# Kernel optimization log

Measured on AMD Instinct MI355X. Metric: run time of the kernel, lower is better.

The kernel has to match this reference:

```python
import jax, jax.numpy as jnp
import numpy as np

B, T, L, D, H = 8, 8192, 256, 512, 8
HD = D // H  # head_dim = 64


def setup_inputs() -> dict:
    key = jax.random.key(0)
    ks = jax.random.split(key, 6)
    s = 0.02
    return {
        "x": jax.random.normal(ks[0], (B, T, D), jnp.float32),
        "query": jax.random.normal(ks[1], (B, L, D), jnp.float32),
        "Wq": jax.random.normal(ks[2], (D, D), jnp.float32) * s,
        "bq": jnp.zeros((D,), jnp.float32),
        "Wkv": jax.random.normal(ks[3], (D, 2 * D), jnp.float32) * s,
        "bkv": jnp.zeros((2 * D,), jnp.float32),
        "Wproj": jax.random.normal(ks[4], (D, D), jnp.float32) * s,
        "bproj": jnp.zeros((D,), jnp.float32),
    }


def reference(x, query, Wq, bq, Wkv, bkv, Wproj, bproj):
    scale = HD ** (-0.5)
    # projections (weights stored [in, out]; equivalent to torch Linear with W.T)
    q = (query @ Wq + bq).reshape(B, L, H, HD).transpose(0, 2, 1, 3)   # [B,H,L,hd]
    kv = (x @ Wkv + bkv).reshape(B, T, 2, H, HD)
    k = kv[:, :, 0].transpose(0, 2, 1, 3)                              # [B,H,T,hd]
    v = kv[:, :, 1].transpose(0, 2, 1, 3)                              # [B,H,T,hd]
    # scaled dot-product attention, full L x T scores as in original
    attn = jnp.einsum("bhld,bhtd->bhlt", q * scale, k)                 # [B,H,L,T]
    attn = jax.nn.softmax(attn, axis=-1)
    out = jnp.einsum("bhlt,bhtd->bhld", attn, v)                       # [B,H,L,hd]
    out = out.transpose(0, 2, 1, 3).reshape(B, L, D)
    return out @ Wproj + bproj
```

## Files before the change

kernel.cpp:

```cpp
#include <hip/hip_runtime.h>
#include <hip/hip_bf16.h>
#include <cstdint>
#include <cstddef>

typedef __bf16 bf16_t;
typedef __bf16 bf16x8 __attribute__((ext_vector_type(8)));
typedef __bf16 bf16x4 __attribute__((ext_vector_type(4)));
typedef float  f32x4  __attribute__((ext_vector_type(4)));

#define DEVI __device__ __forceinline__

constexpr int B_ = 8, T_ = 8192, L_ = 256, D_ = 512, H_ = 8, HD_ = 64;
constexpr float SCALE_LOG2E = 0.125f * 1.44269504088896340736f;
constexpr int NSPLIT = 8;

DEVI void async16(void* lds_base, const void* gptr, int lane) {
#if __has_builtin(__builtin_amdgcn_global_load_lds)
  __builtin_amdgcn_global_load_lds(
      (__attribute__((address_space(1))) void*)gptr,
      (__attribute__((address_space(3))) void*)lds_base, 16, 0, 0);
  (void)lane;
#else
  ((bf16x8*)lds_base)[lane] = *(const bf16x8*)gptr;
#endif
}

__global__ __launch_bounds__(256) void cvt_f32_to_bf16(
    const float* __restrict__ in, bf16_t* __restrict__ out, int n4) {
  int stride = gridDim.x * blockDim.x;
  for (int i = blockIdx.x * blockDim.x + threadIdx.x; i < n4; i += stride) {
    float4 v = ((const float4*)in)[i];
    bf16x4 o;
    o[0] = (bf16_t)v.x; o[1] = (bf16_t)v.y; o[2] = (bf16_t)v.z; o[3] = (bf16_t)v.w;
    ((bf16x4*)out)[i] = o;
  }
}

__global__ __launch_bounds__(256) void transpose_cvt(
    const float* __restrict__ W, bf16_t* __restrict__ WT, int K, int N, float scale) {
  __shared__ float tile[32][33];
  const int tx = threadIdx.x & 31, ty = threadIdx.x >> 5;
  const int n0 = blockIdx.x * 32, k0 = blockIdx.y * 32;
#pragma unroll
  for (int i = 0; i < 4; ++i)
    tile[ty + i * 8][tx] = W[(size_t)(k0 + ty + i * 8) * N + n0 + tx];
  __syncthreads();
#pragma unroll
  for (int i = 0; i < 4; ++i)
    WT[(size_t)(n0 + ty + i * 8) * K + k0 + tx] = (bf16_t)(tile[tx][ty + i * 8] * scale);
}

template <int MODE>
__global__ __launch_bounds__(256, 2) void gemm_bf16(
    const bf16_t* __restrict__ A, const bf16_t* __restrict__ BT,
    const float* __restrict__ bias, float bscale,
    bf16_t* __restrict__ out0, bf16_t* __restrict__ out1,
    float* __restrict__ outf) {
  constexpr int K = 512;
  __shared__ __align__(16) bf16_t As[128 * 32];
  __shared__ __align__(16) bf16_t Bs[128 * 32];
  __shared__ __align__(16) bf16_t Cs[128 * 136];

  const int tid = threadIdx.x;
  const int w = tid >> 6, lane = tid & 63;
  const int m0 = (MODE == 1 ? blockIdx.y : blockIdx.x) * 128;
  const int n0 = (MODE == 1 ? blockIdx.x : blockIdx.y) * 128;
  const int wm = w & 1, wn = w >> 1;

  f32x4 acc[4][4] = {};

  const int srow = w * 32 + (lane >> 2);
  const int scol = (lane & 3) * 8;
  const bf16_t* aG = A + (size_t)(m0 + srow) * K + scol;
  const bf16_t* bG = BT + (size_t)(n0 + srow) * K + scol;
  bf16_t* aL = &As[(w * 32) * 32];
  bf16_t* bL = &Bs[(w * 32) * 32];

  for (int k0 = 0; k0 < K; k0 += 32) {
    async16(aL,           aG + k0,                 lane);
    async16(aL + 16 * 32, aG + k0 + (size_t)16 * K, lane);
    async16(bL,           bG + k0,                 lane);
    async16(bL + 16 * 32, bG + k0 + (size_t)16 * K, lane);
    __syncthreads();
    bf16x8 af[4], bfr[4];
#pragma unroll
    for (int mt = 0; mt < 4; ++mt)
      af[mt] = *(const bf16x8*)&As[(wm * 64 + mt * 16 + (lane & 15)) * 32 + (lane >> 4) * 8];
#pragma unroll
    for (int nt = 0; nt < 4; ++nt)
      bfr[nt] = *(const bf16x8*)&Bs[(wn * 64 + nt * 16 + (lane & 15)) * 32 + (lane >> 4) * 8];
#pragma unroll
    for (int mt = 0; mt < 4; ++mt)
#pragma unroll
      for (int nt = 0; nt < 4; ++nt)
        acc[mt][nt] = __builtin_amdgcn_mfma_f32_16x16x32_bf16(af[mt], bfr[nt], acc[mt][nt], 0, 0, 0);
    __syncthreads();
  }

  if (MODE == 2) {
#pragma unroll
    for (int nt = 0; nt < 4; ++nt) {
      const int col = n0 + wn * 64 + nt * 16 + (lane & 15);
      const float bv = bias[col];
#pragma unroll
      for (int mt = 0; mt < 4; ++mt)
#pragma unroll
        for (int r = 0; r < 4; ++r) {
          const int row = m0 + wm * 64 + mt * 16 + (lane >> 4) * 4 + r;
          outf[(size_t)row * D_ + col] = acc[mt][nt][r] + bv;
        }
    }
    return;
  }

  const bool vside = (MODE == 1) && (n0 >= 512);

#pragma unroll
  for (int nt = 0; nt < 4; ++nt) {
    const int col = wn * 64 + nt * 16 + (lane & 15);
    const float bv = bias[n0 + col] * bscale;
#pragma unroll
    for (int mt = 0; mt < 4; ++mt)
#pragma unroll
      for (int r = 0; r < 4; ++r) {
        const int row = wm * 64 + mt * 16 + (lane >> 4) * 4 + r;
        if (vside) Cs[col * 136 + row] = (bf16_t)(acc[mt][nt][r] + bv);
        else       Cs[row * 136 + col] = (bf16_t)(acc[mt][nt][r] + bv);
      }
  }
  __syncthreads();

  if (MODE == 0) {
#pragma unroll
    for (int i = 0; i < 8; ++i) {
      const int c = tid + i * 256;
      const int row = c >> 4, col = (c & 15) * 8;
      const int gr = m0 + row;
      const int b = gr >> 8, l = gr & 255;
      const int h = (n0 + col) >> 6, hd = (n0 + col) & 63;
      *(float4*)&out0[((size_t)(b * 8 + h) * L_ + l) * 64 + hd] =
          *(const float4*)&Cs[row * 136 + col];
    }
  } else if (!vside) {
#pragma unroll
    for (int i = 0; i < 8; ++i) {
      const int c = tid + i * 256;
      const int row = c >> 4, col = (c & 15) * 8;
      const int gr = m0 + row;
      const int b = gr >> 13, t = gr & 8191;
      const int h = (n0 + col) >> 6, hd = (n0 + col) & 63;
      *(float4*)&out0[((size_t)(b * 8 + h) * T_ + t) * 64 + hd] =
          *(const float4*)&Cs[row * 136 + col];
    }
  } else {
    const int b = m0 >> 13, t0 = m0 & 8191;
#pragma unroll
    for (int i = 0; i < 8; ++i) {
      const int c = tid + i * 256;
      const int tc = c & 15, ch = c >> 4;
      const int h = (n0 - 512 + ch) >> 6, hd = ch & 63;
      *(float4*)&out1[((size_t)(b * 8 + h) * 64 + hd) * T_ + t0 + tc * 8] =
          *(const float4*)&Cs[ch * 136 + tc * 8];
    }
  }
}

__global__ __launch_bounds__(256) void attn_fwd(
    const bf16_t* __restrict__ qg, const bf16_t* __restrict__ kg,
    const bf16_t* __restrict__ vg, float* __restrict__ Opart,
    float* __restrict__ mlbuf) {
  __shared__ __align__(16) char smem[16384 + 16384 + 20480];
  bf16_t* Ks = (bf16_t*)smem;
  bf16_t* Vs = (bf16_t*)(smem + 16384);
  bf16_t* Ps = (bf16_t*)(smem + 32768);
  bf16_t* Qs = Ps;

  const int n = blockIdx.x;
  const int split = n & 7, qt = (n >> 3) & 3, bh = n >> 5;
  const int tid = threadIdx.x;
  const int w = tid >> 6, lane = tid & 63;

  {
    const bf16_t* src = qg + ((size_t)bh * L_ + qt * 64) * 64;
    const int row = w * 16 + (lane >> 2);
#pragma unroll
    for (int hh = 0; hh < 2; ++hh)
      async16(&Qs[hh * 2048 + (w * 16) * 32],
              src + (size_t)row * 64 + hh * 32 + (lane & 3) * 8, lane);
  }
  __syncthreads();

  bf16x8 aq[2];
#pragma unroll
  for (int hh = 0; hh < 2; ++hh)
    aq[hh] = *(const bf16x8*)&Qs[hh * 2048 + (w * 16 + (lane & 15)) * 32 + (lane >> 4) * 8];

  float m_run[4], l_run[4];
  f32x4 O[4] = {};
#pragma unroll
  for (int r = 0; r < 4; ++r) { m_run[r] = -INFINITY; l_run[r] = 0.f; }

  const int kt0 = split * (T_ / 128 / NSPLIT);
  for (int kt = kt0; kt < kt0 + T_ / 128 / NSPLIT; ++kt) {
#pragma unroll
    for (int hh = 0; hh < 2; ++hh)
#pragma unroll
      for (int i = 0; i < 2; ++i) {
        const int trow = kt * 128 + w * 32 + i * 16 + (lane >> 2);
        async16(&Ks[hh * 4096 + (w * 32 + i * 16) * 32],
                kg + ((size_t)bh * T_ + trow) * 64 + hh * 32 + (lane & 3) * 8, lane);
      }
#pragma unroll
    for (int kc = 0; kc < 4; ++kc) {
      const int hd = w * 16 + (lane >> 2);
      async16(&Vs[kc * 2048 + (w * 16) * 32],
              vg + ((size_t)bh * 64 + hd) * T_ + kt * 128 + kc * 32 + (lane & 3) * 8, lane);
    }
    __syncthreads();

    f32x4 S[8];
#pragma unroll
    for (int nt = 0; nt < 8; ++nt) {
      bf16x8 b0 = *(const bf16x8*)&Ks[0 * 4096 + (nt * 16 + (lane & 15)) * 32 + (lane >> 4) * 8];
      bf16x8 b1 = *(const bf16x8*)&Ks[1 * 4096 + (nt * 16 + (lane & 15)) * 32 + (lane >> 4) * 8];
      f32x4 s = {0.f, 0.f, 0.f, 0.f};
      s = __builtin_amdgcn_mfma_f32_16x16x32_bf16(aq[0], b0, s, 0, 0, 0);
      s = __builtin_amdgcn_mfma_f32_16x16x32_bf16(aq[1], b1, s, 0, 0, 0);
      S[nt] = s;
    }

    float alpha[4];
#pragma unroll
    for (int r = 0; r < 4; ++r) {
      float mx = S[0][r];
#pragma unroll
      for (int nt = 1; nt < 8; ++nt) mx = fmaxf(mx, S[nt][r]);
      mx = fmaxf(mx, __shfl_xor(mx, 1));
      mx = fmaxf(mx, __shfl_xor(mx, 2));
      mx = fmaxf(mx, __shfl_xor(mx, 4));
      mx = fmaxf(mx, __shfl_xor(mx, 8));
      const float mnew = fmaxf(m_run[r], mx);
      alpha[r] = exp2f(m_run[r] - mnew);
      m_run[r] = mnew;
      float rs = 0.f;
#pragma unroll
      for (int nt = 0; nt < 8; ++nt) {
        const float p = exp2f(S[nt][r] - mnew);
        S[nt][r] = p;
        rs += p;
      }
      rs += __shfl_xor(rs, 1);
      rs += __shfl_xor(rs, 2);
      rs += __shfl_xor(rs, 4);
      rs += __shfl_xor(rs, 8);
      l_run[r] = alpha[r] * l_run[r] + rs;
    }

#pragma unroll
    for (int nt = 0; nt < 8; ++nt)
#pragma unroll
      for (int r = 0; r < 4; ++r) {
        const int rp = w * 16 + (lane >> 4) * 4 + r;
        const int cf = (nt & 1) * 16 + (lane & 15);
        Ps[(nt >> 1) * 2560 + rp * 40 + (cf ^ (((rp >> 3) & 1) * 16))] = (bf16_t)S[nt][r];
      }

#pragma unroll
    for (int n2 = 0; n2 < 4; ++n2)
#pragma unroll
      for (int r = 0; r < 4; ++r) O[n2][r] *= alpha[r];

    __syncthreads();

#pragma unroll
    for (int kc = 0; kc < 4; ++kc) {
      const int rp = w * 16 + (lane & 15);
      const int cg = ((lane >> 4) * 8) ^ (((rp >> 3) & 1) * 16);
      bf16x8 ap = *(const bf16x8*)&Ps[kc * 2560 + rp * 40 + cg];
#pragma unroll
      for (int n2 = 0; n2 < 4; ++n2) {
        bf16x8 bv = *(const bf16x8*)&Vs[kc * 2048 + (n2 * 16 + (lane & 15)) * 32 + (lane >> 4) * 8];
        O[n2] = __builtin_amdgcn_mfma_f32_16x16x32_bf16(ap, bv, O[n2], 0, 0, 0);
      }
    }
    __syncthreads();
  }

  const int part = ((bh * 4 + qt) * NSPLIT + split);
  float* op = Opart + (size_t)part * 64 * 64;
#pragma unroll
  for (int n2 = 0; n2 < 4; ++n2) {
#pragma unroll
    for (int r = 0; r < 4; ++r) {
      const int row = w * 16 + (lane >> 4) * 4 + r;
      op[(size_t)row * 64 + n2 * 16 + (lane & 15)] = O[n2][r];
    }
  }
  if ((lane & 15) == 0) {
    float* mlb = mlbuf + (size_t)part * 128;
#pragma unroll
    for (int r = 0; r < 4; ++r) {
      const int row = w * 16 + (lane >> 4) * 4 + r;
      mlb[row] = m_run[r];
      mlb[64 + row] = l_run[r];
    }
  }
}

__global__ __launch_bounds__(256) void attn_combine(
    const float* __restrict__ Opart, const float* __restrict__ mlbuf,
    bf16_t* __restrict__ og) {
  const int blk = blockIdx.x;
  const int bh = blk >> 2, qt = blk & 3;
  const int tid = threadIdx.x;
  const int row = tid >> 2, c0 = (tid & 3) * 16;
  const float* mlb = mlbuf + (size_t)blk * NSPLIT * 128;
  float m[NSPLIT], l[NSPLIT], wgt[NSPLIT];
  float M = -INFINITY;
#pragma unroll
  for (int s = 0; s < NSPLIT; ++s) {
    m[s] = mlb[s * 128 + row];
    l[s] = mlb[s * 128 + 64 + row];
    M = fmaxf(M, m[s]);
  }
  float Ls = 0.f;
#pragma unroll
  for (int s = 0; s < NSPLIT; ++s) { wgt[s] = exp2f(m[s] - M); Ls += l[s] * wgt[s]; }
  const float inv = 1.f / Ls;
  f32x4 acc[4] = {};
  const float* ob = Opart + (size_t)blk * NSPLIT * 4096 + row * 64 + c0;
#pragma unroll
  for (int s = 0; s < NSPLIT; ++s)
#pragma unroll
    for (int j = 0; j < 4; ++j) {
      f32x4 v = *(const f32x4*)&ob[s * 4096 + j * 4];
      acc[j] += wgt[s] * v;
    }
  const int b = bh >> 3, h = bh & 7;
  bf16_t* dst = og + ((size_t)(b * L_ + qt * 64 + row)) * D_ + h * 64 + c0;
#pragma unroll
  for (int j = 0; j < 4; ++j) {
    bf16x4 o;
#pragma unroll
    for (int e = 0; e < 4; ++e) o[e] = (bf16_t)(acc[j][e] * inv);
    *(bf16x4*)&dst[j * 4] = o;
  }
}

extern "C" void kernel_launch(void* const* d_in, const int* in_sizes, int n_in,
                              void* d_out, int out_size, void* d_ws, size_t ws_size,
                              hipStream_t stream) {
  const float* x     = (const float*)d_in[0];
  const float* query = (const float*)d_in[1];
  const float* Wq    = (const float*)d_in[2];
  const float* bq    = (const float*)d_in[3];
  const float* Wkv   = (const float*)d_in[4];
  const float* bkv   = (const float*)d_in[5];
  const float* Wproj = (const float*)d_in[6];
  const float* bproj = (const float*)d_in[7];
  float* out = (float*)d_out;

  char* ws = (char*)d_ws;
  bf16_t* xb   = (bf16_t*)(ws + 0);
  float*  Opart = (float*)(ws + 0);
  float*  mlbuf = (float*)(ws + 34603008);
  bf16_t* wkvT = (bf16_t*)(ws + 67108864);
  bf16_t* wqT  = (bf16_t*)(ws + 68157440);
  bf16_t* qin  = (bf16_t*)(ws + 68681728);
  bf16_t* qh   = (bf16_t*)(ws + 70778880);
  bf16_t* kh   = (bf16_t*)(ws + 72876032);
  bf16_t* vTh  = (bf16_t*)(ws + 139984896);
  bf16_t* attnb = (bf16_t*)(ws + 207093760);
  bf16_t* wprojT = (bf16_t*)(ws + 209190912);

  cvt_f32_to_bf16<<<4096, 256, 0, stream>>>(x, xb, (B_ * T_ * D_) / 4);
  cvt_f32_to_bf16<<<1024, 256, 0, stream>>>(query, qin, (B_ * L_ * D_) / 4);
  transpose_cvt<<<dim3(16, 16), 256, 0, stream>>>(Wq, wqT, 512, 512, SCALE_LOG2E);
  transpose_cvt<<<dim3(32, 16), 256, 0, stream>>>(Wkv, wkvT, 512, 1024, 1.0f);
  transpose_cvt<<<dim3(16, 16), 256, 0, stream>>>(Wproj, wprojT, 512, 512, 1.0f);
  gemm_bf16<0><<<dim3(16, 4), 256, 0, stream>>>(qin, wqT, bq, SCALE_LOG2E, qh, nullptr, nullptr);
  gemm_bf16<1><<<dim3(8, 512), 256, 0, stream>>>(xb, wkvT, bkv, 1.0f, kh, vTh, nullptr);
  attn_fwd<<<dim3(64 * 4 * NSPLIT), 256, 0, stream>>>(qh, kh, vTh, Opart, mlbuf);
  attn_combine<<<dim3(256), 256, 0, stream>>>(Opart, mlbuf, attnb);
  gemm_bf16<2><<<dim3(16, 4), 256, 0, stream>>>(attnb, wprojT, bproj, 1.0f, nullptr, nullptr, out);
}
```

Measured before the change: 470.8 us.

## Shrink LDS footprints, raise occupancy, double attention split count, widen GEMM K-step

The GEMM now stages 64-wide K slices with an XOR swizzle and puts the staging buffers and the epilogue C tile in one LDS union. That lets launch bounds allow 4 blocks per CU, and the KV GEMM grid is reordered so the M tiles vary fastest. Attention aliases the Q, K and P buffers into one LDS region with a new swizzle and adds barriers to keep that safe, targets 5 blocks per CU, and raises NSPLIT from 8 to 16 for more parallelism. The trade-off is extra barriers, more partial outputs for the combine step, and the m/l buffer moved to a new workspace offset.

```diff
diff --git a/kernel.cpp b/kernel.cpp
--- a/kernel.cpp
+++ b/kernel.cpp
@@ -12,7 +12,7 @@
 
 constexpr int B_ = 8, T_ = 8192, L_ = 256, D_ = 512, H_ = 8, HD_ = 64;
 constexpr float SCALE_LOG2E = 0.125f * 1.44269504088896340736f;
-constexpr int NSPLIT = 8;
+constexpr int NSPLIT = 16;
 
 DEVI void async16(void* lds_base, const void* gptr, int lane) {
 #if __has_builtin(__builtin_amdgcn_global_load_lds)
@@ -51,49 +51,53 @@
 }
 
 template <int MODE>
-__global__ __launch_bounds__(256, 2) void gemm_bf16(
+__global__ __launch_bounds__(256, 4) void gemm_bf16(
     const bf16_t* __restrict__ A, const bf16_t* __restrict__ BT,
     const float* __restrict__ bias, float bscale,
     bf16_t* __restrict__ out0, bf16_t* __restrict__ out1,
     float* __restrict__ outf) {
   constexpr int K = 512;
-  __shared__ __align__(16) bf16_t As[128 * 32];
-  __shared__ __align__(16) bf16_t Bs[128 * 32];
-  __shared__ __align__(16) bf16_t Cs[128 * 136];
+  __shared__ __align__(16) union SM {
+    bf16_t stage[2][128 * 64];
+    bf16_t cs[128 * 136];
+  } sm;
 
   const int tid = threadIdx.x;
   const int w = tid >> 6, lane = tid & 63;
-  const int m0 = (MODE == 1 ? blockIdx.y : blockIdx.x) * 128;
-  const int n0 = (MODE == 1 ? blockIdx.x : blockIdx.y) * 128;
+  const int m0 = blockIdx.x * 128, n0 = blockIdx.y * 128;
   const int wm = w & 1, wn = w >> 1;
 
   f32x4 acc[4][4] = {};
 
-  const int srow = w * 32 + (lane >> 2);
-  const int scol = (lane & 3) * 8;
-  const bf16_t* aG = A + (size_t)(m0 + srow) * K + scol;
-  const bf16_t* bG = BT + (size_t)(n0 + srow) * K + scol;
-  bf16_t* aL = &As[(w * 32) * 32];
-  bf16_t* bL = &Bs[(w * 32) * 32];
-
-  for (int k0 = 0; k0 < K; k0 += 32) {
-    async16(aL,           aG + k0,                 lane);
-    async16(aL + 16 * 32, aG + k0 + (size_t)16 * K, lane);
-    async16(bL,           bG + k0,                 lane);
-    async16(bL + 16 * 32, bG + k0 + (size_t)16 * K, lane);
-    __syncthreads();
-    bf16x8 af[4], bfr[4];
-#pragma unroll
-    for (int mt = 0; mt < 4; ++mt)
-      af[mt] = *(const bf16x8*)&As[(wm * 64 + mt * 16 + (lane & 15)) * 32 + (lane >> 4) * 8];
-#pragma unroll
-    for (int nt = 0; nt < 4; ++nt)
-      bfr[nt] = *(const bf16x8*)&Bs[(wn * 64 + nt * 16 + (lane & 15)) * 32 + (lane >> 4) * 8];
-#pragma unroll
-    for (int mt = 0; mt < 4; ++mt)
+  const int sw = ((lane & 7) ^ ((lane >> 3) & 7)) * 8;
+  const bf16_t* aG = A + (size_t)(m0 + w * 32 + (lane >> 3)) * K + sw;
+  const bf16_t* bG = BT + (size_t)(n0 + w * 32 + (lane >> 3)) * K + sw;
+  bf16_t* aL = &sm.stage[0][(w * 32) * 64];
+  bf16_t* bL = &sm.stage[1][(w * 32) * 64];
+
+  for (int k0 = 0; k0 < K; k0 += 64) {
+#pragma unroll
+    for (int i = 0; i < 4; ++i) {
+      async16(aL + i * (8 * 64), aG + k0 + (size_t)(i * 8) * K, lane);
+      async16(bL + i * (8 * 64), bG + k0 + (size_t)(i * 8) * K, lane);
+    }
+    __syncthreads();
+#pragma unroll
+    for (int kk = 0; kk < 2; ++kk) {
+      bf16x8 af[4], bfr[4];
+      const int cc = ((kk * 4 + (lane >> 4)) ^ (lane & 7)) * 8;
+#pragma unroll
+      for (int mt = 0; mt < 4; ++mt)
+        af[mt] = *(const bf16x8*)&sm.stage[0][(wm * 64 + mt * 16 + (lane & 15)) * 64 + cc];
 #pragma unroll
       for (int nt = 0; nt < 4; ++nt)
-        acc[mt][nt] = __builtin_amdgcn_mfma_f32_16x16x32_bf16(af[mt], bfr[nt], acc[mt][nt], 0, 0, 0);
+        bfr[nt] = *(const bf16x8*)&sm.stage[1][(wn * 64 + nt * 16 + (lane & 15)) * 64 + cc];
+#pragma unroll
+      for (int mt = 0; mt < 4; ++mt)
+#pragma unroll
+        for (int nt = 0; nt < 4; ++nt)
+          acc[mt][nt] = __builtin_amdgcn_mfma_f32_16x16x32_bf16(af[mt], bfr[nt], acc[mt][nt], 0, 0, 0);
+    }
     __syncthreads();
   }
 
@@ -124,8 +128,8 @@
 #pragma unroll
       for (int r = 0; r < 4; ++r) {
         const int row = wm * 64 + mt * 16 + (lane >> 4) * 4 + r;
-        if (vside) Cs[col * 136 + row] = (bf16_t)(acc[mt][nt][r] + bv);
-        else       Cs[row * 136 + col] = (bf16_t)(acc[mt][nt][r] + bv);
+        if (vside) sm.cs[col * 136 + row] = (bf16_t)(acc[mt][nt][r] + bv);
+        else       sm.cs[row * 136 + col] = (bf16_t)(acc[mt][nt][r] + bv);
       }
   }
   __syncthreads();
@@ -139,7 +143,7 @@
       const int b = gr >> 8, l = gr & 255;
       const int h = (n0 + col) >> 6, hd = (n0 + col) & 63;
       *(float4*)&out0[((size_t)(b * 8 + h) * L_ + l) * 64 + hd] =
-          *(const float4*)&Cs[row * 136 + col];
+          *(const float4*)&sm.cs[row * 136 + col];
     }
   } else if (!vside) {
 #pragma unroll
@@ -150,7 +154,7 @@
       const int b = gr >> 13, t = gr & 8191;
       const int h = (n0 + col) >> 6, hd = (n0 + col) & 63;
       *(float4*)&out0[((size_t)(b * 8 + h) * T_ + t) * 64 + hd] =
-          *(const float4*)&Cs[row * 136 + col];
+          *(const float4*)&sm.cs[row * 136 + col];
     }
   } else {
     const int b = m0 >> 13, t0 = m0 & 8191;
@@ -160,23 +164,23 @@
       const int tc = c & 15, ch = c >> 4;
       const int h = (n0 - 512 + ch) >> 6, hd = ch & 63;
       *(float4*)&out1[((size_t)(b * 8 + h) * 64 + hd) * T_ + t0 + tc * 8] =
-          *(const float4*)&Cs[ch * 136 + tc * 8];
-    }
-  }
-}
-
-__global__ __launch_bounds__(256) void attn_fwd(
+          *(const float4*)&sm.cs[ch * 136 + tc * 8];
+    }
+  }
+}
+
+__global__ __launch_bounds__(256, 5) void attn_fwd(
     const bf16_t* __restrict__ qg, const bf16_t* __restrict__ kg,
     const bf16_t* __restrict__ vg, float* __restrict__ Opart,
     float* __restrict__ mlbuf) {
-  __shared__ __align__(16) char smem[16384 + 16384 + 20480];
-  bf16_t* Ks = (bf16_t*)smem;
-  bf16_t* Vs = (bf16_t*)(smem + 16384);
-  bf16_t* Ps = (bf16_t*)(smem + 32768);
-  bf16_t* Qs = Ps;
+  __shared__ __align__(16) bf16_t KPs[2 * 128 * 32];
+  __shared__ __align__(16) bf16_t Vs[4 * 64 * 32];
+  bf16_t* Ks = KPs;
+  bf16_t* Ps = KPs;
+  bf16_t* Qs = KPs;
 
   const int n = blockIdx.x;
-  const int split = n & 7, qt = (n >> 3) & 3, bh = n >> 5;
+  const int split = n & 15, qt = (n >> 4) & 3, bh = n >> 6;
   const int tid = threadIdx.x;
   const int w = tid >> 6, lane = tid & 63;
 
@@ -194,6 +198,7 @@
 #pragma unroll
   for (int hh = 0; hh < 2; ++hh)
     aq[hh] = *(const bf16x8*)&Qs[hh * 2048 + (w * 16 + (lane & 15)) * 32 + (lane >> 4) * 8];
+  __syncthreads();
 
   float m_run[4], l_run[4];
   f32x4 O[4] = {};
@@ -256,13 +261,15 @@
       l_run[r] = alpha[r] * l_run[r] + rs;
     }
 
+    __syncthreads();
+
 #pragma unroll
     for (int nt = 0; nt < 8; ++nt)
 #pragma unroll
       for (int r = 0; r < 4; ++r) {
         const int rp = w * 16 + (lane >> 4) * 4 + r;
-        const int cf = (nt & 1) * 16 + (lane & 15);
-        Ps[(nt >> 1) * 2560 + rp * 40 + (cf ^ (((rp >> 3) & 1) * 16))] = (bf16_t)S[nt][r];
+        const int cf = ((nt & 1) * 16 + (lane & 15)) ^ (((rp >> 2) & 1) * 16);
+        Ps[(nt >> 1) * 2048 + rp * 32 + cf] = (bf16_t)S[nt][r];
       }
 
 #pragma unroll
@@ -275,8 +282,8 @@
 #pragma unroll
     for (int kc = 0; kc < 4; ++kc) {
       const int rp = w * 16 + (lane & 15);
-      const int cg = ((lane >> 4) * 8) ^ (((rp >> 3) & 1) * 16);
-      bf16x8 ap = *(const bf16x8*)&Ps[kc * 2560 + rp * 40 + cg];
+      const int cg = ((lane >> 4) * 8) ^ (((rp >> 2) & 1) * 16);
+      bf16x8 ap = *(const bf16x8*)&Ps[kc * 2048 + rp * 32 + cg];
 #pragma unroll
       for (int n2 = 0; n2 < 4; ++n2) {
         bf16x8 bv = *(const bf16x8*)&Vs[kc * 2048 + (n2 * 16 + (lane & 15)) * 32 + (lane >> 4) * 8];
@@ -363,7 +370,6 @@
   char* ws = (char*)d_ws;
   bf16_t* xb   = (bf16_t*)(ws + 0);
   float*  Opart = (float*)(ws + 0);
-  float*  mlbuf = (float*)(ws + 34603008);
   bf16_t* wkvT = (bf16_t*)(ws + 67108864);
   bf16_t* wqT  = (bf16_t*)(ws + 68157440);
   bf16_t* qin  = (bf16_t*)(ws + 68681728);
@@ -372,6 +378,7 @@
   bf16_t* vTh  = (bf16_t*)(ws + 139984896);
   bf16_t* attnb = (bf16_t*)(ws + 207093760);
   bf16_t* wprojT = (bf16_t*)(ws + 209190912);
+  float*  mlbuf = (float*)(ws + 209715200);
 
   cvt_f32_to_bf16<<<4096, 256, 0, stream>>>(x, xb, (B_ * T_ * D_) / 4);
   cvt_f32_to_bf16<<<1024, 256, 0, stream>>>(query, qin, (B_ * L_ * D_) / 4);
@@ -379,7 +386,7 @@
   transpose_cvt<<<dim3(32, 16), 256, 0, stream>>>(Wkv, wkvT, 512, 1024, 1.0f);
   transpose_cvt<<<dim3(16, 16), 256, 0, stream>>>(Wproj, wprojT, 512, 512, 1.0f);
   gemm_bf16<0><<<dim3(16, 4), 256, 0, stream>>>(qin, wqT, bq, SCALE_LOG2E, qh, nullptr, nullptr);
-  gemm_bf16<1><<<dim3(8, 512), 256, 0, stream>>>(xb, wkvT, bkv, 1.0f, kh, vTh, nullptr);
+  gemm_bf16<1><<<dim3(512, 8), 256, 0, stream>>>(xb, wkvT, bkv, 1.0f, kh, vTh, nullptr);
   attn_fwd<<<dim3(64 * 4 * NSPLIT), 256, 0, stream>>>(qh, kh, vTh, Opart, mlbuf);
   attn_combine<<<dim3(256), 256, 0, stream>>>(Opart, mlbuf, attnb);
   gemm_bf16<2><<<dim3(16, 4), 256, 0, stream>>>(attnb, wprojT, bproj, 1.0f, nullptr, nullptr, out);
```

Measured after the change: 462.5 us. No clear change (-1.8%).
